# Kernel tuning notes

Measured on AMD Instinct MI355X. Metric: run time of the kernel, lower is better.

## Reference

```python
import jax, jax.numpy as jnp
import numpy as np
import math

PHI = (1.0 + math.sqrt(5.0)) / 2.0
KAPPA = 0.5
B_, L_, D_, N_, R_ = 4, 1024, 768, 16, 48  # batch, seq, d_model, state_size, dt_rank


@jax.custom_vjp
def fractal_pow(mag, exponent):
    # |h|^e with torch _FractalCompress semantics (clamped-ratio grad, no grad wrt e)
    return jnp.maximum(mag, 1e-8) ** exponent


def _fp_fwd(mag, exponent):
    mag_safe = jnp.maximum(mag, 1e-8)
    compressed = mag_safe ** exponent
    ratio = exponent * compressed / (mag_safe + 1e-10)
    return compressed, ratio


def _fp_bwd(ratio, g):
    return (g * jnp.minimum(ratio, 5.0), jnp.zeros_like(ratio))


fractal_pow.defvjp(_fp_fwd, _fp_bwd)


def setup_inputs() -> dict:
    key = jax.random.key(0)
    ks = jax.random.split(key, 7)

    def u(k, shape, fan_in):
        b = (1.0 / PHI) / math.sqrt(fan_in)
        return jax.random.uniform(k, shape, jnp.float32, -b, b)

    x = jax.random.normal(ks[0], (B_, L_, D_), dtype=jnp.float32)
    in_proj_w = u(ks[1], (D_, 2 * D_), D_)          # Linear(D, 2D, bias=False), stored (in,out)
    x_proj_w = u(ks[2], (D_, R_ + 4 * N_), D_)      # Linear(D, dt_rank + 2*N*2, bias=False)
    dt_proj_w = u(ks[3], (R_, D_), R_)              # Linear(dt_rank, D)
    bb = 1.0 / math.sqrt(R_)
    dt_proj_b = jax.random.uniform(ks[4], (D_,), jnp.float32, -bb, bb)
    out_proj_w = u(ks[5], (D_, D_), D_)             # Linear(D, D)
    ob = 1.0 / math.sqrt(D_)
    out_proj_b = jax.random.uniform(ks[6], (D_,), jnp.float32, -ob, ob)
    # phi-scaled A init (exact torch init)
    n_slow = round(N_ / PHI)
    n_fast = N_ - n_slow
    A_init = np.concatenate([np.linspace(0.5, 2.0, n_slow), np.linspace(2.0, float(N_), n_fast)])
    A_log = jnp.asarray(np.log(A_init), dtype=jnp.float32)
    return dict(x=x, in_proj_w=in_proj_w, x_proj_w=x_proj_w, dt_proj_w=dt_proj_w,
                dt_proj_b=dt_proj_b, out_proj_w=out_proj_w, out_proj_b=out_proj_b, A_log=A_log)


def _forward(x, in_proj_w, x_proj_w, dt_proj_w, dt_proj_b, out_proj_w, out_proj_b, A_log):
    B, L, D = x.shape
    N = A_log.shape[0]
    R = dt_proj_w.shape[0]

    xz = x @ in_proj_w                               # (B,L,2D)
    x_in = jax.nn.silu(xz[..., :D])
    z = xz[..., D:]
    xp = x_in @ x_proj_w                             # (B,L,R+4N)
    dt = jax.nn.softplus(xp[..., :R] @ dt_proj_w + dt_proj_b)  # (B,L,D)
    bc = xp[..., R:].reshape(B, L, 2, N, 2)
    Bm, Cm = bc[:, :, 0], bc[:, :, 1]                # (B,L,N,2) each

    # dna_init: 16 phases, magnitude 0.01
    phases = jnp.linspace(0.0, 2.0 * math.pi * (1.0 - 1.0 / N), N)
    h0 = 0.01 * jnp.stack([jnp.cos(phases), jnp.sin(phases)], axis=-1)  # (N,2)
    h0 = jnp.broadcast_to(h0, (B, D, N, 2)) + jnp.zeros((B, D, N, 2), jnp.float32)
    A_neg = -jnp.exp(A_log)                          # (N,)

    def step(h, inp):
        x_t, dt_t, Bt, Ct = inp                      # (B,D),(B,D),(B,N,2),(B,N,2)
        alpha = jnp.exp(dt_t[..., None] * A_neg)     # (B,D,N)
        e = 1.0 + (1.0 - alpha) * KAPPA
        # fractal compress: |h|^e, phase preserved
        mag = jnp.sqrt(h[..., 0] ** 2 + h[..., 1] ** 2 + 1e-8)
        ph = jnp.arctan2(h[..., 1], h[..., 0] + 1e-10)
        cm = fractal_pow(mag, e)
        h = jnp.stack([cm * jnp.cos(ph), cm * jnp.sin(ph)], axis=-1)
        # h += gamma * B * x  (x is real, so complex mul is a scale of B)
        h = h + Bt[:, None, :, :] * (x_t * dt_t)[:, :, None, None]
        # tanh magnitude squash, phase preserved
        m2 = jnp.sqrt(h[..., 0] ** 2 + h[..., 1] ** 2 + 1e-8)
        p2 = jnp.arctan2(h[..., 1], h[..., 0] + 1e-10)
        s = jnp.tanh(m2)
        h = jnp.stack([s * jnp.cos(p2), s * jnp.sin(p2)], axis=-1)
        # y = Re(conj(C) * h).sum(N) = C_re*h_re + C_im*h_im summed over N
        y = jnp.sum(Ct[:, None, :, 0] * h[..., 0] + Ct[:, None, :, 1] * h[..., 1], axis=-1)
        return h, y

    xs = (x_in.swapaxes(0, 1), dt.swapaxes(0, 1), Bm.swapaxes(0, 1), Cm.swapaxes(0, 1))
    _, ys = jax.lax.scan(step, h0, xs)               # ys: (L,B,D)
    y = ys.swapaxes(0, 1) * jax.nn.silu(z)
    return y @ out_proj_w + out_proj_b


def reference(x, in_proj_w, x_proj_w, dt_proj_w, dt_proj_b, out_proj_w, out_proj_b, A_log):
    return _forward(x, in_proj_w, x_proj_w, dt_proj_w, dt_proj_b, out_proj_w, out_proj_b, A_log)
```

## Files before the change

### kernel.cpp

```cpp
#include <hip/hip_runtime.h>
#include <math.h>

#if __has_builtin(__builtin_amdgcn_exp2f)
#define EXP2F(x) __builtin_amdgcn_exp2f(x)
#else
#define EXP2F(x) exp2f(x)
#endif
#if __has_builtin(__builtin_amdgcn_logf)
#define LOG2F(x) __builtin_amdgcn_logf(x)
#else
#define LOG2F(x) log2f(x)
#endif
#if __has_builtin(__builtin_amdgcn_rcpf)
#define RCPF(x) __builtin_amdgcn_rcpf(x)
#else
#define RCPF(x) (1.0f / (x))
#endif

#define LOG2E 1.4426950408889634f

typedef __bf16 bf16x8 __attribute__((ext_vector_type(8)));
typedef float f32x4 __attribute__((ext_vector_type(4)));

__device__ __forceinline__ float silu_f(float v) {
    return v * RCPF(1.0f + EXP2F(-v * LOG2E));
}
__device__ __forceinline__ float softplus_f(float v) {
    return fmaxf(v, 0.0f) + log1pf(__expf(-fabsf(v)));
}

template <int CTRL>
__device__ __forceinline__ float dpp_add(float v) {
    int r = __builtin_amdgcn_update_dpp(0, __float_as_int(v), CTRL, 0xF, 0xF, true);
    return v + __int_as_float(r);
}

__device__ __forceinline__ unsigned short bf16_rne(float f) {
    unsigned int u = __float_as_uint(f);
    return (unsigned short)((u + 0x7FFFu + ((u >> 16) & 1u)) >> 16);
}
__device__ __forceinline__ unsigned short bf16_hi(float f, float& rem) {
    unsigned int u = __float_as_uint(f);
    unsigned int hb = (u + 0x7FFFu + ((u >> 16) & 1u)) >> 16;
    rem = f - __uint_as_float(hb << 16);
    return (unsigned short)hb;
}

__device__ __forceinline__ void async_g2l16(const void* g, void* l) {
    __builtin_amdgcn_global_load_lds(
        (const __attribute__((address_space(1))) unsigned int*)g,
        (__attribute__((address_space(3))) unsigned int*)l, 16, 0, 0);
}

__global__ __launch_bounds__(256) void conv_all_k(
    const float* __restrict__ x,
    unsigned short* __restrict__ xh,
    const float* __restrict__ w_in,
    unsigned short* __restrict__ wih, unsigned short* __restrict__ wil,
    const float* __restrict__ w_out,
    unsigned short* __restrict__ woh, unsigned short* __restrict__ wol,
    const float* __restrict__ w_xp,
    const float* __restrict__ w_dt,
    const float* __restrict__ b_dt,
    unsigned short* __restrict__ wbh, unsigned short* __restrict__ wbl,
    float* __restrict__ bias_full)
{
    __shared__ float shmem[6272];
    const int bid = blockIdx.x;
    const int t = threadIdx.x;
    if (bid < 3072) {
        int i = bid * 256 + t;
        float4 v = ((const float4*)x)[i];
        ushort4 h;
        h.x = bf16_rne(v.x);
        h.y = bf16_rne(v.y);
        h.z = bf16_rne(v.z);
        h.w = bf16_rne(v.w);
        ((ushort4*)xh)[i] = h;
        return;
    }
    if (bid < 4800) {
        const float* W;
        unsigned short *Th, *Tl;
        int N, bx, by;
        if (bid < 4224) {
            int b2 = bid - 3072;
            W = w_in; Th = wih; Tl = wil; N = 1536;
            bx = b2 % 48; by = b2 / 48;
        } else {
            int b3 = bid - 4224;
            W = w_out; Th = woh; Tl = wol; N = 768;
            bx = b3 % 24; by = b3 / 24;
        }
        const int K = 768;
        float (*tile)[33] = (float (*)[33])shmem;
        const int tx = t & 31, ty = t >> 5;
        const int n0 = bx * 32, k0 = by * 32;
#pragma unroll
        for (int r = 0; r < 4; ++r)
            tile[ty + r * 8][tx] = W[(size_t)(k0 + ty + r * 8) * N + n0 + tx];
        __syncthreads();
#pragma unroll
        for (int r = 0; r < 4; ++r) {
            float v = tile[tx][ty + r * 8];
            float rem;
            unsigned short h = bf16_hi(v, rem);
            size_t o = (size_t)(n0 + ty + r * 8) * K + k0 + tx;
            Th[o] = h;
            Tl[o] = bf16_rne(rem);
        }
        return;
    }
    if (bid < 4944) {
        int b4 = bid - 4800;
        int bxw = b4 % 12, byw = b4 / 12;
        const int kd0 = byw * 64, dd0 = bxw * 64;
        float* As = shmem;
        float* Ws = shmem + 64 * 49;
        {
            int r = t >> 2;
            int c4 = (t & 3) * 4;
#pragma unroll
            for (int s = 0; s < 3; ++s) {
                float4 a = *(const float4*)&w_xp[(size_t)(kd0 + r) * 112 + c4 + 16 * s];
                As[r * 49 + c4 + 16 * s + 0] = a.x;
                As[r * 49 + c4 + 16 * s + 1] = a.y;
                As[r * 49 + c4 + 16 * s + 2] = a.z;
                As[r * 49 + c4 + 16 * s + 3] = a.w;
            }
            int rw = t >> 4;
            int cw = (t & 15) * 4;
#pragma unroll
            for (int s = 0; s < 3; ++s) {
                float4 w = *(const float4*)&w_dt[(size_t)(rw + 16 * s) * 768 + dd0 + cw];
                Ws[(rw + 16 * s) * 65 + cw + 0] = w.x;
                Ws[(rw + 16 * s) * 65 + cw + 1] = w.y;
                Ws[(rw + 16 * s) * 65 + cw + 2] = w.z;
                Ws[(rw + 16 * s) * 65 + cw + 3] = w.w;
            }
        }
        __syncthreads();
        const int ty = t >> 4, tx = t & 15;
        float acc[4][4];
#pragma unroll
        for (int i = 0; i < 4; ++i)
#pragma unroll
            for (int j = 0; j < 4; ++j) acc[i][j] = 0.0f;
        for (int k = 0; k < 48; ++k) {
            float ar[4], wr[4];
#pragma unroll
            for (int i = 0; i < 4; ++i) ar[i] = As[(ty * 4 + i) * 49 + k];
#pragma unroll
            for (int j = 0; j < 4; ++j) wr[j] = Ws[k * 65 + tx * 4 + j];
#pragma unroll
            for (int i = 0; i < 4; ++i)
#pragma unroll
                for (int j = 0; j < 4; ++j)
                    acc[i][j] = fmaf(ar[i], wr[j], acc[i][j]);
        }
        __syncthreads();
        float* Ot = shmem;
#pragma unroll
        for (int i = 0; i < 4; ++i)
#pragma unroll
            for (int j = 0; j < 4; ++j)
                Ot[(tx * 4 + j) * 65 + ty * 4 + i] = acc[i][j];
        __syncthreads();
        int dl = t >> 2, c0 = (t & 3) * 16;
#pragma unroll
        for (int k = 0; k < 16; ++k) {
            float v = Ot[dl * 65 + c0 + k];
            float rem;
            unsigned short h = bf16_hi(v, rem);
            size_t o = (size_t)(64 + dd0 + dl) * 768 + kd0 + c0 + k;
            wbh[o] = h;
            wbl[o] = bf16_rne(rem);
        }
        return;
    }
    if (bid < 4992) {
        int b5 = bid - 4944;
        int bxb = b5 & 1, byb = b5 >> 1;
        const int n0 = bxb * 32, k0 = byb * 32;
        float (*tile)[33] = (float (*)[33])shmem;
        const int tx = t & 31, ty = t >> 5;
#pragma unroll
        for (int r = 0; r < 4; ++r)
            tile[ty + r * 8][tx] = w_xp[(size_t)(k0 + ty + r * 8) * 112 + 48 + n0 + tx];
        __syncthreads();
#pragma unroll
        for (int r = 0; r < 4; ++r) {
            float v = tile[tx][ty + r * 8];
            float rem;
            unsigned short h = bf16_hi(v, rem);
            size_t o = (size_t)(n0 + ty + r * 8) * 768 + k0 + tx;
            wbh[o] = h;
            wbl[o] = bf16_rne(rem);
        }
        return;
    }
#pragma unroll
    for (int i = 0; i < 4; ++i) {
        int idx = t + 256 * i;
        if (idx < 896)
            bias_full[idx] = (idx >= 64 && idx < 832) ? b_dt[idx - 64] : 0.0f;
    }
}

template <int EPI, int WRX>
__global__ __launch_bounds__(256, 3) void mgemm_k(
    const unsigned short* __restrict__ Ah,
    const unsigned short* __restrict__ Bth, const unsigned short* __restrict__ Btl,
    const float* __restrict__ bias,
    float* __restrict__ C, int K, int ldc, int nby,
    unsigned short* __restrict__ xh, unsigned short* __restrict__ xl)
{
    __shared__ unsigned short smem[3 * 4096];

    const int t = threadIdx.x;
    const int wave = t >> 6, lane = t & 63;
    const int bx = blockIdx.x / nby, by = blockIdx.x % nby;
    const int bm = by * 128, bn = bx * 128;
    const int mw = (wave >> 1) * 64, nw = (wave & 1) * 64;

    const unsigned short* smat;
    int row0, ninst;
    char* lmat;
    if      (wave == 0) { smat = Ah;  row0 = bm;      ninst = 4; lmat = (char*)smem; }
    else if (wave == 1) { smat = Ah;  row0 = bm + 64; ninst = 4; lmat = (char*)smem + 4096; }
    else if (wave == 2) { smat = Bth; row0 = bn;      ninst = 8; lmat = (char*)(smem + 4096); }
    else                { smat = Btl; row0 = bn;      ninst = 8; lmat = (char*)(smem + 8192); }
    const int lr = lane >> 2;
    const int kq = (lane & 3) ^ ((lane >> 3) & 3);
    const unsigned short* gbase = smat + (size_t)(row0 + lr) * K + kq * 8;

    const int la = lane & 15, g4 = lane >> 4;
    const int fo = (g4 ^ ((la >> 1) & 3)) * 8;
    const int aoff = (mw + la) * 32 + fo;
    const int boff = (nw + la) * 32 + fo;
    const unsigned short* pAh = smem + aoff;
    const unsigned short* pBh = smem + 4096 + boff;
    const unsigned short* pBl = smem + 8192 + boff;

    f32x4 acc[4][4];
#pragma unroll
    for (int i = 0; i < 4; ++i)
#pragma unroll
        for (int j = 0; j < 4; ++j) acc[i][j] = (f32x4){0.f, 0.f, 0.f, 0.f};

    for (int k0 = 0; k0 < K; k0 += 32) {
        const unsigned short* g = gbase + k0;
        if (ninst == 4) {
#pragma unroll
            for (int j = 0; j < 4; ++j)
                async_g2l16(g + (size_t)j * 16 * K, lmat + j * 1024);
        } else {
#pragma unroll
            for (int j = 0; j < 8; ++j)
                async_g2l16(g + (size_t)j * 16 * K, lmat + j * 1024);
        }
        __syncthreads();

        bf16x8 fah[4], fbh[4], fbl[4];
#pragma unroll
        for (int i = 0; i < 4; ++i) {
            fah[i] = *(const bf16x8*)(pAh + i * 512);
            fbh[i] = *(const bf16x8*)(pBh + i * 512);
            fbl[i] = *(const bf16x8*)(pBl + i * 512);
        }
#pragma unroll
        for (int i = 0; i < 4; ++i)
#pragma unroll
            for (int j = 0; j < 4; ++j)
                acc[i][j] = __builtin_amdgcn_mfma_f32_16x16x32_bf16(fah[i], fbh[j], acc[i][j], 0, 0, 0);
#pragma unroll
        for (int i = 0; i < 4; ++i)
#pragma unroll
            for (int j = 0; j < 4; ++j)
                acc[i][j] = __builtin_amdgcn_mfma_f32_16x16x32_bf16(fah[i], fbl[j], acc[i][j], 0, 0, 0);
        __syncthreads();
    }

#pragma unroll
    for (int i = 0; i < 4; ++i) {
        int row = bm + mw + i * 16 + g4 * 4;
#pragma unroll
        for (int j = 0; j < 4; ++j) {
            int col = bn + nw + j * 16 + la;
            float bz = bias ? bias[col] : 0.0f;
#pragma unroll
            for (int r = 0; r < 4; ++r) {
                float v = acc[i][j][r] + bz;
                if (EPI == 1) v = silu_f(v);
                C[(size_t)(row + r) * ldc + col] = v;
                if (WRX) {
                    if (col < 768) {
                        float rem;
                        unsigned short hh = bf16_hi(v, rem);
                        xh[(size_t)(row + r) * 768 + col] = hh;
                        xl[(size_t)(row + r) * 768 + col] = bf16_rne(rem);
                    }
                }
            }
        }
    }
}

__global__ __launch_bounds__(256, 3) void mgemm3_k(
    const unsigned short* __restrict__ Ahp, const unsigned short* __restrict__ Alp,
    const unsigned short* __restrict__ Bth, const unsigned short* __restrict__ Btl,
    const float* __restrict__ bias,
    float* __restrict__ C, int K, int ldc, int nby)
{
    __shared__ unsigned short smem[4 * 4096];

    const int t = threadIdx.x;
    const int wave = t >> 6, lane = t & 63;
    const int bx = blockIdx.x / nby, by = blockIdx.x % nby;
    const int bm = by * 128, bn = bx * 128;
    const int mw = (wave >> 1) * 64, nw = (wave & 1) * 64;

    const unsigned short* smat;
    int row0;
    char* lmat;
    if      (wave == 0) { smat = Ahp; row0 = bm; lmat = (char*)smem; }
    else if (wave == 1) { smat = Alp; row0 = bm; lmat = (char*)(smem + 4096); }
    else if (wave == 2) { smat = Bth; row0 = bn; lmat = (char*)(smem + 8192); }
    else                { smat = Btl; row0 = bn; lmat = (char*)(smem + 12288); }
    const int lr = lane >> 2;
    const int kq = (lane & 3) ^ ((lane >> 3) & 3);
    const unsigned short* gbase = smat + (size_t)(row0 + lr) * K + kq * 8;

    const int la = lane & 15, g4 = lane >> 4;
    const int fo = (g4 ^ ((la >> 1) & 3)) * 8;
    const int aoff = (mw + la) * 32 + fo;
    const int boff = (nw + la) * 32 + fo;
    const unsigned short* pAh = smem + aoff;
    const unsigned short* pAl = smem + 4096 + aoff;
    const unsigned short* pBh = smem + 8192 + boff;
    const unsigned short* pBl = smem + 12288 + boff;

    f32x4 acc[4][4];
#pragma unroll
    for (int i = 0; i < 4; ++i)
#pragma unroll
        for (int j = 0; j < 4; ++j) acc[i][j] = (f32x4){0.f, 0.f, 0.f, 0.f};

    for (int k0 = 0; k0 < K; k0 += 32) {
        const unsigned short* g = gbase + k0;
#pragma unroll
        for (int j = 0; j < 8; ++j)
            async_g2l16(g + (size_t)j * 16 * K, lmat + j * 1024);
        __syncthreads();

        bf16x8 fah[4], fal[4], fbh[4], fbl[4];
#pragma unroll
        for (int i = 0; i < 4; ++i) {
            fah[i] = *(const bf16x8*)(pAh + i * 512);
            fal[i] = *(const bf16x8*)(pAl + i * 512);
            fbh[i] = *(const bf16x8*)(pBh + i * 512);
            fbl[i] = *(const bf16x8*)(pBl + i * 512);
        }
#pragma unroll
        for (int i = 0; i < 4; ++i)
#pragma unroll
            for (int j = 0; j < 4; ++j)
                acc[i][j] = __builtin_amdgcn_mfma_f32_16x16x32_bf16(fah[i], fbh[j], acc[i][j], 0, 0, 0);
#pragma unroll
        for (int i = 0; i < 4; ++i)
#pragma unroll
            for (int j = 0; j < 4; ++j)
                acc[i][j] = __builtin_amdgcn_mfma_f32_16x16x32_bf16(fah[i], fbl[j], acc[i][j], 0, 0, 0);
#pragma unroll
        for (int i = 0; i < 4; ++i)
#pragma unroll
            for (int j = 0; j < 4; ++j)
                acc[i][j] = __builtin_amdgcn_mfma_f32_16x16x32_bf16(fal[i], fbh[j], acc[i][j], 0, 0, 0);
        __syncthreads();
    }

#pragma unroll
    for (int i = 0; i < 4; ++i) {
        int row = bm + mw + i * 16 + g4 * 4;
#pragma unroll
        for (int j = 0; j < 4; ++j) {
            int col = bn + nw + j * 16 + la;
            float bz = bias[col];
#pragma unroll
            for (int r = 0; r < 4; ++r) {
                float v = acc[i][j][r] + bz;
                if (col >= 64) v = softplus_f(v);
                C[(size_t)(row + r) * ldc + col] = v;
            }
        }
    }
}

#define L_LEN 1024
#define CH 32
#define NCH (L_LEN / CH)
#define CHP (CH + 4)

__global__ __launch_bounds__(512) void scan_k(
    const float* __restrict__ xz,
    const float* __restrict__ bcdt,
    const float* __restrict__ A_log,
    unsigned short* __restrict__ ybh)
{
    __shared__ float xdt_t[2][16][CHP];
    __shared__ float ds_t[2][16][CHP];
    __shared__ float B0s[2][16][CHP];
    __shared__ float B1s[2][16][CHP];
    __shared__ float C0s[2][16][CHP];
    __shared__ float C1s[2][16][CHP];
    __shared__ float ysp[2][CH][16][4];

    const int t  = threadIdx.x;
    const int b  = blockIdx.y;
    const int d0 = blockIdx.x * 16;
    const size_t rowbase = (size_t)b * L_LEN;
    const bool is_chain = (t < 256);

    const int n  = t & 15;
    const int dl = (t >> 4) & 15;
    const int ng = n >> 2;
    float negAl2e = 0.0f, h0 = 0.0f, h1 = 0.0f;
    float s2 = 1.0f, lT = 0.0f;
    if (is_chain) {
        negAl2e = -__expf(A_log[n]) * LOG2E;
        float phase = 6.283185307179586f * (float)n / 16.0f;
        h0 = 0.01f * cosf(phase);
        h1 = 0.01f * sinf(phase);
        lT = LOG2F(fmaf(h0, h0, fmaf(h1, h1, 1e-8f)));
    }

    const int t2 = t - 256;
    const int hl = t2 >> 2;
    const int hf = (t2 & 3) * 4;

    auto stage = [&](int cc) {
        const int bi = cc & 1;
        if (t2 < 128) {
            size_t row = rowbase + cc * CH + hl;
            float4 rx = *(const float4*)&xz[row * 1536 + d0 + hf];
            float4 rd = *(const float4*)&bcdt[row * 896 + 64 + d0 + hf];
            xdt_t[bi][hf + 0][hl] = rx.x * rd.x;
            xdt_t[bi][hf + 1][hl] = rx.y * rd.y;
            xdt_t[bi][hf + 2][hl] = rx.z * rd.z;
            xdt_t[bi][hf + 3][hl] = rx.w * rd.w;
            ds_t[bi][hf + 0][hl] = rd.x;
            ds_t[bi][hf + 1][hl] = rd.y;
            ds_t[bi][hf + 2][hl] = rd.z;
            ds_t[bi][hf + 3][hl] = rd.w;
        }
#pragma unroll
        for (int i = 0; i < 2; ++i) {
            int idx = t2 + 256 * i;
            int lb = idx >> 4, j4 = (idx & 15) * 4;
            float4 rbc = *(const float4*)&bcdt[(rowbase + cc * CH + lb) * 896 + j4];
            if (j4 < 32) {
                int nn = j4 >> 1;
                B0s[bi][nn][lb]     = rbc.x;
                B1s[bi][nn][lb]     = rbc.y;
                B0s[bi][nn + 1][lb] = rbc.z;
                B1s[bi][nn + 1][lb] = rbc.w;
            } else {
                int nn = (j4 - 32) >> 1;
                C0s[bi][nn][lb]     = rbc.x;
                C1s[bi][nn][lb]     = rbc.y;
                C0s[bi][nn + 1][lb] = rbc.z;
                C1s[bi][nn + 1][lb] = rbc.w;
            }
        }
    };

    auto store_y = [&](int cs) {
        if (t2 >= 128) return;
        const int bi = cs & 1;
        size_t row = rowbase + cs * CH + hl;
        float4 zq = *(const float4*)&xz[row * 1536 + 768 + d0 + hf];
        float yr[4];
#pragma unroll
        for (int j = 0; j < 4; ++j) {
            float4 p = *(const float4*)&ysp[bi][hl][hf + j][0];
            yr[j] = (p.x + p.y) + (p.z + p.w);
        }
        ushort4 hh;
        hh.x = bf16_rne(yr[0] * zq.x);
        hh.y = bf16_rne(yr[1] * zq.y);
        hh.z = bf16_rne(yr[2] * zq.z);
        hh.w = bf16_rne(yr[3] * zq.w);
        *(ushort4*)&ybh[row * 768 + d0 + hf] = hh;
    };

    if (!is_chain) stage(0);
    __syncthreads();

    for (int c = 0; c < NCH; ++c) {
        if (is_chain) {
            const int bi = c & 1;
            const float* xr  = &xdt_t[bi][dl][0];
            const float* dr  = &ds_t[bi][dl][0];
            const float* b0r = &B0s[bi][n][0];
            const float* b1r = &B1s[bi][n][0];
            const float* c0r = &C0s[bi][n][0];
            const float* c1r = &C1s[bi][n][0];

            float4 px  = *(const float4*)(xr);
            float4 pd  = *(const float4*)(dr);
            float4 pb0 = *(const float4*)(b0r);
            float4 pb1 = *(const float4*)(b1r);
            float4 pc0 = *(const float4*)(c0r);
            float4 pc1 = *(const float4*)(c1r);

            for (int l4 = 0; l4 < CH; l4 += 4) {
                float4 cx = px, cd = pd, cb0 = pb0, cb1 = pb1, cc0 = pc0, cc1 = pc1;
                if (l4 + 4 < CH) {
                    px  = *(const float4*)(xr  + l4 + 4);
                    pd  = *(const float4*)(dr  + l4 + 4);
                    pb0 = *(const float4*)(b0r + l4 + 4);
                    pb1 = *(const float4*)(b1r + l4 + 4);
                    pc0 = *(const float4*)(c0r + l4 + 4);
                    pc1 = *(const float4*)(c1r + l4 + 4);
                }
                const float xv[4]  = {cx.x,  cx.y,  cx.z,  cx.w};
                const float dv[4]  = {cd.x,  cd.y,  cd.z,  cd.w};
                const float C0v[4] = {cc0.x, cc0.y, cc0.z, cc0.w};
                const float C1v[4] = {cc1.x, cc1.y, cc1.z, cc1.w};

                float cfv[4], bx0[4], bx1[4];
                const float B0v[4] = {cb0.x, cb0.y, cb0.z, cb0.w};
                const float B1v[4] = {cb1.x, cb1.y, cb1.z, cb1.w};
#pragma unroll
                for (int u = 0; u < 4; ++u) {
                    cfv[u] = fmaf(EXP2F(dv[u] * negAl2e), -0.25f, 0.25f);
                    bx0[u] = B0v[u] * xv[u];
                    bx1[u] = B1v[u] * xv[u];
                }

#pragma unroll
                for (int u = 0; u < 4; ++u) {
                    float g = s2 * EXP2F(cfv[u] * lT);
                    h0 = fmaf(h0, g, bx0[u]);
                    h1 = fmaf(h1, g, bx1[u]);
                    float q  = fmaf(h0, h0, fmaf(h1, h1, 1e-8f));
                    float q2 = q * q;
                    float num = fmaf(q2, q + 378.0f,              fmaf(17325.0f, q, 135135.0f));
                    float den = fmaf(q2, fmaf(28.0f, q, 3150.0f), fmaf(62370.0f, q, 135135.0f));
                    s2 = num * RCPF(den);
                    lT = LOG2F(s2 * s2 * q);

                    float yv = s2 * fmaf(C0v[u], h0, C1v[u] * h1);
                    yv = dpp_add<0xB1>(yv);
                    yv = dpp_add<0x4E>(yv);
                    if ((n & 3) == 0) ysp[bi][l4 + u][dl][ng] = yv;
                }
            }
        } else {
            if (c + 1 < NCH) stage(c + 1);
            if (c >= 1) store_y(c - 1);
        }
        __syncthreads();
    }
    if (!is_chain) store_y(NCH - 1);
}

extern "C" void kernel_launch(void* const* d_in, const int* in_sizes, int n_in,
                              void* d_out, int out_size, void* d_ws, size_t ws_size,
                              hipStream_t stream)
{
    const float* x     = (const float*)d_in[0];
    const float* w_in  = (const float*)d_in[1];
    const float* w_xp  = (const float*)d_in[2];
    const float* w_dt  = (const float*)d_in[3];
    const float* b_dt  = (const float*)d_in[4];
    const float* w_out = (const float*)d_in[5];
    const float* b_out = (const float*)d_in[6];
    const float* A_log = (const float*)d_in[7];
    float* out = (float*)d_out;

    const int M = 4096;
    float* xz        = (float*)d_ws;
    float* bcdt      = xz + (size_t)M * 1536;
    float* bias_full = bcdt + (size_t)M * 896;
    unsigned short* ah   = (unsigned short*)(bias_full + 896);
    unsigned short* ybh  = ah   + (size_t)M * 768;
    unsigned short* xinh = ybh  + (size_t)M * 768;
    unsigned short* xinl = xinh + (size_t)M * 768;
    unsigned short* wh   = xinl + (size_t)M * 768;
    unsigned short* wl   = wh   + (size_t)1536 * 768;
    unsigned short* voh  = wl   + (size_t)1536 * 768;
    unsigned short* vol  = voh  + (size_t)768 * 768;
    unsigned short* wbh  = vol  + (size_t)768 * 768;
    unsigned short* wbl  = wbh  + (size_t)896 * 768;

    dim3 blk(256);

    conv_all_k<<<dim3(4993), blk, 0, stream>>>(
        x, ah, w_in, wh, wl, w_out, voh, vol,
        w_xp, w_dt, b_dt, wbh, wbl, bias_full);

    mgemm_k<1, 1><<<dim3(12 * 32), blk, 0, stream>>>(
        ah, wh, wl, (const float*)nullptr, xz, 768, 1536, 32, xinh, xinl);

    mgemm3_k<<<dim3(7 * 32), blk, 0, stream>>>(
        xinh, xinl, wbh, wbl, bias_full, bcdt, 768, 896, 32);

    scan_k<<<dim3(48, 4), dim3(512), 0, stream>>>(xz, bcdt, A_log, ybh);

    mgemm_k<0, 0><<<dim3(6 * 32), blk, 0, stream>>>(
        ybh, voh, vol, b_out, out, 768, 768, 32,
        (unsigned short*)nullptr, (unsigned short*)nullptr);
}
```

Before: 310.6 us.

## Double-buffer GEMM LDS tiles, batch x conversion, trim scan reduction, raise chain priority

Both split-bf16 GEMM kernels now double-buffer their LDS tiles: the next K-slice is issued asynchronously before the current one is consumed, with an explicit vmcnt drain before the barrier. Occupancy hints drop from 3 to 2 blocks per CU to make room for the doubled shared memory. The conversion kernel handles four x chunks per block, cutting the grid from 4993 to 2689 blocks. In the scan, the recurrence chain drops one DPP reduction step and leaves eight partials per row for the store path to sum, and it raises its wave priority while running. Together these aim to hide global-load latency and shorten the serial chain, at the cost of lower GEMM occupancy and more LDS traffic in the scan.

```diff
diff --git a/kernel.cpp b/kernel.cpp
--- a/kernel.cpp
+++ b/kernel.cpp
@@ -18,6 +18,8 @@
 #endif
 
 #define LOG2E 1.4426950408889634f
+
+#define DRAIN_VMEM() asm volatile("s_waitcnt vmcnt(0)" ::: "memory")
 
 typedef __bf16 bf16x8 __attribute__((ext_vector_type(8)));
 typedef float f32x4 __attribute__((ext_vector_type(4)));
@@ -68,27 +70,30 @@
     __shared__ float shmem[6272];
     const int bid = blockIdx.x;
     const int t = threadIdx.x;
-    if (bid < 3072) {
-        int i = bid * 256 + t;
-        float4 v = ((const float4*)x)[i];
-        ushort4 h;
-        h.x = bf16_rne(v.x);
-        h.y = bf16_rne(v.y);
-        h.z = bf16_rne(v.z);
-        h.w = bf16_rne(v.w);
-        ((ushort4*)xh)[i] = h;
+    if (bid < 768) {
+#pragma unroll
+        for (int r = 0; r < 4; ++r) {
+            int i = (bid + 768 * r) * 256 + t;
+            float4 v = ((const float4*)x)[i];
+            ushort4 h;
+            h.x = bf16_rne(v.x);
+            h.y = bf16_rne(v.y);
+            h.z = bf16_rne(v.z);
+            h.w = bf16_rne(v.w);
+            ((ushort4*)xh)[i] = h;
+        }
         return;
     }
-    if (bid < 4800) {
+    if (bid < 2496) {
         const float* W;
         unsigned short *Th, *Tl;
         int N, bx, by;
-        if (bid < 4224) {
-            int b2 = bid - 3072;
+        if (bid < 1920) {
+            int b2 = bid - 768;
             W = w_in; Th = wih; Tl = wil; N = 1536;
             bx = b2 % 48; by = b2 / 48;
         } else {
-            int b3 = bid - 4224;
+            int b3 = bid - 1920;
             W = w_out; Th = woh; Tl = wol; N = 768;
             bx = b3 % 24; by = b3 / 24;
         }
@@ -111,8 +116,8 @@
         }
         return;
     }
-    if (bid < 4944) {
-        int b4 = bid - 4800;
+    if (bid < 2640) {
+        int b4 = bid - 2496;
         int bxw = b4 % 12, byw = b4 / 12;
         const int kd0 = byw * 64, dd0 = bxw * 64;
         float* As = shmem;
@@ -178,8 +183,8 @@
         }
         return;
     }
-    if (bid < 4992) {
-        int b5 = bid - 4944;
+    if (bid < 2688) {
+        int b5 = bid - 2640;
         int bxb = b5 & 1, byb = b5 >> 1;
         const int n0 = bxb * 32, k0 = byb * 32;
         float (*tile)[33] = (float (*)[33])shmem;
@@ -208,14 +213,14 @@
 }
 
 template <int EPI, int WRX>
-__global__ __launch_bounds__(256, 3) void mgemm_k(
+__global__ __launch_bounds__(256, 2) void mgemm_k(
     const unsigned short* __restrict__ Ah,
     const unsigned short* __restrict__ Bth, const unsigned short* __restrict__ Btl,
     const float* __restrict__ bias,
     float* __restrict__ C, int K, int ldc, int nby,
     unsigned short* __restrict__ xh, unsigned short* __restrict__ xl)
 {
-    __shared__ unsigned short smem[3 * 4096];
+    __shared__ unsigned short smem[2][3 * 4096];
 
     const int t = threadIdx.x;
     const int wave = t >> 6, lane = t & 63;
@@ -225,11 +230,11 @@
 
     const unsigned short* smat;
     int row0, ninst;
-    char* lmat;
-    if      (wave == 0) { smat = Ah;  row0 = bm;      ninst = 4; lmat = (char*)smem; }
-    else if (wave == 1) { smat = Ah;  row0 = bm + 64; ninst = 4; lmat = (char*)smem + 4096; }
-    else if (wave == 2) { smat = Bth; row0 = bn;      ninst = 8; lmat = (char*)(smem + 4096); }
-    else                { smat = Btl; row0 = bn;      ninst = 8; lmat = (char*)(smem + 8192); }
+    int lmoff;
+    if      (wave == 0) { smat = Ah;  row0 = bm;      ninst = 4; lmoff = 0; }
+    else if (wave == 1) { smat = Ah;  row0 = bm + 64; ninst = 4; lmoff = 4096; }
+    else if (wave == 2) { smat = Bth; row0 = bn;      ninst = 8; lmoff = 8192; }
+    else                { smat = Btl; row0 = bn;      ninst = 8; lmoff = 16384; }
     const int lr = lane >> 2;
     const int kq = (lane & 3) ^ ((lane >> 3) & 3);
     const unsigned short* gbase = smat + (size_t)(row0 + lr) * K + kq * 8;
@@ -238,9 +243,6 @@
     const int fo = (g4 ^ ((la >> 1) & 3)) * 8;
     const int aoff = (mw + la) * 32 + fo;
     const int boff = (nw + la) * 32 + fo;
-    const unsigned short* pAh = smem + aoff;
-    const unsigned short* pBh = smem + 4096 + boff;
-    const unsigned short* pBl = smem + 8192 + boff;
 
     f32x4 acc[4][4];
 #pragma unroll
@@ -248,18 +250,32 @@
 #pragma unroll
         for (int j = 0; j < 4; ++j) acc[i][j] = (f32x4){0.f, 0.f, 0.f, 0.f};
 
-    for (int k0 = 0; k0 < K; k0 += 32) {
+    auto stage = [&](int buf, int k0) {
+        char* lm = (char*)smem + buf * 24576 + lmoff;
         const unsigned short* g = gbase + k0;
         if (ninst == 4) {
 #pragma unroll
             for (int j = 0; j < 4; ++j)
-                async_g2l16(g + (size_t)j * 16 * K, lmat + j * 1024);
+                async_g2l16(g + (size_t)j * 16 * K, lm + j * 1024);
         } else {
 #pragma unroll
             for (int j = 0; j < 8; ++j)
-                async_g2l16(g + (size_t)j * 16 * K, lmat + j * 1024);
-        }
-        __syncthreads();
+                async_g2l16(g + (size_t)j * 16 * K, lm + j * 1024);
+        }
+    };
+
+    stage(0, 0);
+    DRAIN_VMEM();
+    __syncthreads();
+
+    for (int k0 = 0; k0 < K; k0 += 32) {
+        const int cur = (k0 >> 5) & 1;
+        if (k0 + 32 < K) stage(cur ^ 1, k0 + 32);
+
+        const unsigned short* base = &smem[cur][0];
+        const unsigned short* pAh = base + aoff;
+        const unsigned short* pBh = base + 4096 + boff;
+        const unsigned short* pBl = base + 8192 + boff;
 
         bf16x8 fah[4], fbh[4], fbl[4];
 #pragma unroll
@@ -278,6 +294,7 @@
 #pragma unroll
             for (int j = 0; j < 4; ++j)
                 acc[i][j] = __builtin_amdgcn_mfma_f32_16x16x32_bf16(fah[i], fbl[j], acc[i][j], 0, 0, 0);
+        DRAIN_VMEM();
         __syncthreads();
     }
 
@@ -306,13 +323,13 @@
     }
 }
 
-__global__ __launch_bounds__(256, 3) void mgemm3_k(
+__global__ __launch_bounds__(256, 2) void mgemm3_k(
     const unsigned short* __restrict__ Ahp, const unsigned short* __restrict__ Alp,
     const unsigned short* __restrict__ Bth, const unsigned short* __restrict__ Btl,
     const float* __restrict__ bias,
     float* __restrict__ C, int K, int ldc, int nby)
 {
-    __shared__ unsigned short smem[4 * 4096];
+    __shared__ unsigned short smem[2][4 * 4096];
 
     const int t = threadIdx.x;
     const int wave = t >> 6, lane = t & 63;
@@ -321,12 +338,11 @@
     const int mw = (wave >> 1) * 64, nw = (wave & 1) * 64;
 
     const unsigned short* smat;
-    int row0;
-    char* lmat;
-    if      (wave == 0) { smat = Ahp; row0 = bm; lmat = (char*)smem; }
-    else if (wave == 1) { smat = Alp; row0 = bm; lmat = (char*)(smem + 4096); }
-    else if (wave == 2) { smat = Bth; row0 = bn; lmat = (char*)(smem + 8192); }
-    else                { smat = Btl; row0 = bn; lmat = (char*)(smem + 12288); }
+    int row0, lmoff;
+    if      (wave == 0) { smat = Ahp; row0 = bm; lmoff = 0; }
+    else if (wave == 1) { smat = Alp; row0 = bm; lmoff = 8192; }
+    else if (wave == 2) { smat = Bth; row0 = bn; lmoff = 16384; }
+    else                { smat = Btl; row0 = bn; lmoff = 24576; }
     const int lr = lane >> 2;
     const int kq = (lane & 3) ^ ((lane >> 3) & 3);
     const unsigned short* gbase = smat + (size_t)(row0 + lr) * K + kq * 8;
@@ -335,10 +351,6 @@
     const int fo = (g4 ^ ((la >> 1) & 3)) * 8;
     const int aoff = (mw + la) * 32 + fo;
     const int boff = (nw + la) * 32 + fo;
-    const unsigned short* pAh = smem + aoff;
-    const unsigned short* pAl = smem + 4096 + aoff;
-    const unsigned short* pBh = smem + 8192 + boff;
-    const unsigned short* pBl = smem + 12288 + boff;
 
     f32x4 acc[4][4];
 #pragma unroll
@@ -346,12 +358,27 @@
 #pragma unroll
         for (int j = 0; j < 4; ++j) acc[i][j] = (f32x4){0.f, 0.f, 0.f, 0.f};
 
+    auto stage = [&](int buf, int k0) {
+        char* lm = (char*)smem + buf * 32768 + lmoff;
+        const unsigned short* g = gbase + k0;
+#pragma unroll
+        for (int j = 0; j < 8; ++j)
+            async_g2l16(g + (size_t)j * 16 * K, lm + j * 1024);
+    };
+
+    stage(0, 0);
+    DRAIN_VMEM();
+    __syncthreads();
+
     for (int k0 = 0; k0 < K; k0 += 32) {
-        const unsigned short* g = gbase + k0;
-#pragma unroll
-        for (int j = 0; j < 8; ++j)
-            async_g2l16(g + (size_t)j * 16 * K, lmat + j * 1024);
-        __syncthreads();
+        const int cur = (k0 >> 5) & 1;
+        if (k0 + 32 < K) stage(cur ^ 1, k0 + 32);
+
+        const unsigned short* base = &smem[cur][0];
+        const unsigned short* pAh = base + aoff;
+        const unsigned short* pAl = base + 4096 + aoff;
+        const unsigned short* pBh = base + 8192 + boff;
+        const unsigned short* pBl = base + 12288 + boff;
 
         bf16x8 fah[4], fal[4], fbh[4], fbl[4];
 #pragma unroll
@@ -376,6 +403,7 @@
 #pragma unroll
             for (int j = 0; j < 4; ++j)
                 acc[i][j] = __builtin_amdgcn_mfma_f32_16x16x32_bf16(fal[i], fbh[j], acc[i][j], 0, 0, 0);
+        DRAIN_VMEM();
         __syncthreads();
     }
 
@@ -413,7 +441,7 @@
     __shared__ float B1s[2][16][CHP];
     __shared__ float C0s[2][16][CHP];
     __shared__ float C1s[2][16][CHP];
-    __shared__ float ysp[2][CH][16][4];
+    __shared__ float ysp[2][CH][16][8];
 
     const int t  = threadIdx.x;
     const int b  = blockIdx.y;
@@ -423,7 +451,7 @@
 
     const int n  = t & 15;
     const int dl = (t >> 4) & 15;
-    const int ng = n >> 2;
+    const int np = n >> 1;
     float negAl2e = 0.0f, h0 = 0.0f, h1 = 0.0f;
     float s2 = 1.0f, lT = 0.0f;
     if (is_chain) {
@@ -482,8 +510,9 @@
         float yr[4];
 #pragma unroll
         for (int j = 0; j < 4; ++j) {
-            float4 p = *(const float4*)&ysp[bi][hl][hf + j][0];
-            yr[j] = (p.x + p.y) + (p.z + p.w);
+            float4 p0 = *(const float4*)&ysp[bi][hl][hf + j][0];
+            float4 p1 = *(const float4*)&ysp[bi][hl][hf + j][4];
+            yr[j] = ((p0.x + p0.y) + (p0.z + p0.w)) + ((p1.x + p1.y) + (p1.z + p1.w));
         }
         ushort4 hh;
         hh.x = bf16_rne(yr[0] * zq.x);
@@ -498,6 +527,7 @@
 
     for (int c = 0; c < NCH; ++c) {
         if (is_chain) {
+            __builtin_amdgcn_s_setprio(1);
             const int bi = c & 1;
             const float* xr  = &xdt_t[bi][dl][0];
             const float* dr  = &ds_t[bi][dl][0];
@@ -552,10 +582,10 @@
 
                     float yv = s2 * fmaf(C0v[u], h0, C1v[u] * h1);
                     yv = dpp_add<0xB1>(yv);
-                    yv = dpp_add<0x4E>(yv);
-                    if ((n & 3) == 0) ysp[bi][l4 + u][dl][ng] = yv;
+                    if ((n & 1) == 0) ysp[bi][l4 + u][dl][np] = yv;
                 }
             }
+            __builtin_amdgcn_s_setprio(0);
         } else {
             if (c + 1 < NCH) stage(c + 1);
             if (c >= 1) store_y(c - 1);
@@ -596,7 +626,7 @@
 
     dim3 blk(256);
 
-    conv_all_k<<<dim3(4993), blk, 0, stream>>>(
+    conv_all_k<<<dim3(2689), blk, 0, stream>>>(
         x, ah, w_in, wh, wl, w_out, voh, vol,
         w_xp, w_dt, b_dt, wbh, wbl, bias_full);
 
```

Measured after the change: 275.4 us. 11.3% less time.
